# Performance work log

Measured on AMD Instinct MI355X. Metric: run time of the kernel, lower is better.

Reference implementation:

```python
import jax, jax.numpy as jnp
import numpy as np

N_NODES = 50000
N_EDGES = 800000
N_FEAT, N_HID, N_LATENT = 512, 256, 128


def spmm(rows, cols, vals, dense):
    # out[r] += vals[e] * dense[cols[e]]  -- COO SpMM via segment_sum
    gathered = dense[cols] * vals[:, None]          # [E, d]
    return jax.ops.segment_sum(gathered, rows, num_segments=N_NODES)


def setup_inputs() -> dict:
    key = jax.random.key(0)
    ks = jax.random.split(key, 8)
    x = jax.random.normal(ks[0], (N_NODES, N_FEAT), dtype=jnp.float32)
    edge_rows = jax.random.randint(ks[1], (N_EDGES,), 0, N_NODES, dtype=jnp.int32)
    edge_cols = jax.random.randint(ks[2], (N_EDGES,), 0, N_NODES, dtype=jnp.int32)
    edge_vals = jax.random.uniform(ks[3], (N_EDGES,), dtype=jnp.float32)
    # Glorot-style init like the torch GraphConvolution
    W1 = jax.random.normal(ks[4], (N_FEAT, N_HID), dtype=jnp.float32) / np.sqrt(N_FEAT)
    b1 = jnp.zeros((N_HID,), dtype=jnp.float32)
    W2 = jax.random.normal(ks[5], (N_HID, N_LATENT), dtype=jnp.float32) / np.sqrt(N_HID)
    b2 = jnp.zeros((N_LATENT,), dtype=jnp.float32)
    return {"x": x, "edge_rows": edge_rows, "edge_cols": edge_cols,
            "edge_vals": edge_vals, "W1": W1, "b1": b1, "W2": W2, "b2": b2}


def reference(x, edge_rows, edge_cols, edge_vals, W1, b1, W2, b2):
    # layer 1: relu(adj @ (x @ W1) + b1)
    h = spmm(edge_rows, edge_cols, edge_vals, x @ W1) + b1
    h = jax.nn.relu(h)
    # layer 2: relu(adj @ (h @ W2) + b2)
    z = spmm(edge_rows, edge_cols, edge_vals, h @ W2) + b2
    return jax.nn.relu(z)
```

## Files before the change

kernel.cpp:

```cpp
#include <hip/hip_runtime.h>
#include <hip/hip_bf16.h>


typedef __attribute__((ext_vector_type(8))) short bf16x8;
typedef __attribute__((ext_vector_type(4))) float f32x4;

#define NN 50000
#define NE 800000
#define NF 512
#define NH 256
#define NL 128
#define NB ((NN + 255) / 256)

static __device__ __forceinline__ unsigned short f2bf(float f) {
  union { float f; unsigned int u; } v; v.f = f;
  unsigned int r = v.u + 0x7fffu + ((v.u >> 16) & 1u);
  return (unsigned short)(r >> 16);
}
static __device__ __forceinline__ float bf2f(unsigned short u) {
  union { unsigned int u; float f; } v; v.u = (unsigned int)u << 16;
  return v.f;
}

static __device__ __forceinline__ void gll16(const void* g, void* l) {
  __builtin_amdgcn_global_load_lds(
      (const __attribute__((address_space(1))) void*)g,
      (__attribute__((address_space(3))) void*)l, 16, 0, 0);
}

extern "C" __global__ void k_hist(const int* __restrict__ rows, int* __restrict__ counts, int n) {
  int i = blockIdx.x * 256 + threadIdx.x;
  if (i < n) atomicAdd(&counts[rows[i]], 1);
}

extern "C" __global__ __launch_bounds__(256) void k_blocksum(
    const int* __restrict__ counts, int* __restrict__ bsum, int n) {
  __shared__ int s[256];
  int t = threadIdx.x;
  int i = blockIdx.x * 256 + t;
  s[t] = (i < n) ? counts[i] : 0;
  __syncthreads();
  for (int off = 128; off > 0; off >>= 1) {
    if (t < off) s[t] += s[t + off];
    __syncthreads();
  }
  if (t == 0) bsum[blockIdx.x] = s[0];
}

extern "C" __global__ __launch_bounds__(256) void k_scansums(
    const int* __restrict__ bsum, int* __restrict__ bpre, int* __restrict__ rp, int nb, int n) {
  __shared__ int s[256];
  int t = threadIdx.x;
  int v = (t < nb) ? bsum[t] : 0;
  s[t] = v;
  __syncthreads();
  for (int off = 1; off < 256; off <<= 1) {
    int u = (t >= off) ? s[t - off] : 0;
    __syncthreads();
    s[t] += u;
    __syncthreads();
  }
  if (t < nb) bpre[t] = s[t] - v;
  if (t == 255) rp[n] = s[255];
}

extern "C" __global__ __launch_bounds__(256) void k_scanfin(
    const int* __restrict__ counts, const int* __restrict__ bpre,
    int* __restrict__ rp, int* __restrict__ cur, int n) {
  __shared__ int s[256];
  int t = threadIdx.x;
  int i = blockIdx.x * 256 + t;
  int c = (i < n) ? counts[i] : 0;
  s[t] = c;
  __syncthreads();
  for (int off = 1; off < 256; off <<= 1) {
    int u = (t >= off) ? s[t - off] : 0;
    __syncthreads();
    s[t] += u;
    __syncthreads();
  }
  if (i < n) {
    int e = bpre[blockIdx.x] + s[t] - c;
    rp[i] = e;
    cur[i] = e;
  }
}

extern "C" __global__ void k_scatter(const int* __restrict__ rows, const int* __restrict__ cols,
    const float* __restrict__ vals, int* __restrict__ cur, int2* __restrict__ ep, int n) {
  int i = blockIdx.x * 256 + threadIdx.x;
  if (i < n) {
    int p = atomicAdd(&cur[rows[i]], 1);
    int2 e; e.x = cols[i]; e.y = __float_as_int(vals[i]);
    ep[p] = e;
  }
}

extern "C" __global__ void k_cast4(const float4* __restrict__ in, ushort4* __restrict__ out, int n4) {
  int i = blockIdx.x * 256 + threadIdx.x;
  if (i < n4) {
    float4 f = in[i];
    ushort4 o; o.x = f2bf(f.x); o.y = f2bf(f.y); o.z = f2bf(f.z); o.w = f2bf(f.w);
    out[i] = o;
  }
}

extern "C" __global__ void k_transcast(const float* __restrict__ w, unsigned short* __restrict__ wt,
                                       int K, int N) {
  int k = blockIdx.x; int n = threadIdx.x;
  wt[(size_t)n * K + k] = f2bf(w[(size_t)k * N + n]);
}

#define BM 128
#define BN 128
#define BK 32

extern "C" __global__ __launch_bounds__(256) void k_gemm(
    const unsigned short* __restrict__ A, const unsigned short* __restrict__ BT,
    unsigned short* __restrict__ C, int M, int N, int K) {
  __shared__ __align__(16) unsigned short sA[BM * BK];
  __shared__ __align__(16) unsigned short sB[BN * BK];
  int tid = threadIdx.x;
  int lane = tid & 63, wid = tid >> 6;
  int wm = (wid >> 1) * 64, wn = (wid & 1) * 64;
  int bm = blockIdx.x * BM, bn = blockIdx.y * BN;
  int l15 = lane & 15, lq = lane >> 4;
  f32x4 acc[4][4];
#pragma unroll
  for (int i = 0; i < 4; ++i)
#pragma unroll
    for (int j = 0; j < 4; ++j) acc[i][j] = (f32x4){0.f, 0.f, 0.f, 0.f};

  for (int k0 = 0; k0 < K; k0 += BK) {
#pragma unroll
    for (int i = 0; i < 2; ++i) {
      int u = tid + 256 * i;
      int row = u >> 2, uc = (u & 3) * 8;
      int ga = bm + row; if (ga >= M) ga = M - 1;
      gll16(A + (size_t)ga * K + k0 + uc, &sA[row * BK + uc]);
      int gb = bn + row; if (gb >= N) gb = N - 1;
      gll16(BT + (size_t)gb * K + k0 + uc, &sB[row * BK + uc]);
    }
    __syncthreads();
    bf16x8 af[4], bfr[4];
#pragma unroll
    for (int t = 0; t < 4; ++t) {
      af[t]  = *(const bf16x8*)(&sA[(wm + t * 16 + l15) * BK + lq * 8]);
      bfr[t] = *(const bf16x8*)(&sB[(wn + t * 16 + l15) * BK + lq * 8]);
    }
#pragma unroll
    for (int mt = 0; mt < 4; ++mt)
#pragma unroll
      for (int nt = 0; nt < 4; ++nt)
        acc[mt][nt] = __builtin_amdgcn_mfma_f32_16x16x32_bf16(af[mt], bfr[nt], acc[mt][nt], 0, 0, 0);
    __syncthreads();
  }
#pragma unroll
  for (int mt = 0; mt < 4; ++mt) {
#pragma unroll
    for (int r = 0; r < 4; ++r) {
      int gr = bm + wm + mt * 16 + lq * 4 + r;
      if (gr < M) {
#pragma unroll
        for (int nt = 0; nt < 4; ++nt) {
          int gc = bn + wn + nt * 16 + l15;
          C[(size_t)gr * N + gc] = f2bf(acc[mt][nt][r]);
        }
      }
    }
  }
}

extern "C" __global__ __launch_bounds__(256) void k_spmm256(
    const int* __restrict__ rp, const int2* __restrict__ ep,
    const unsigned short* __restrict__ src, const float* __restrict__ bias,
    ushort4* __restrict__ out) {
  int row = blockIdx.x * 4 + (threadIdx.x >> 6);
  int lane = threadIdx.x & 63;
  if (row >= NN) return;
  int e0 = __builtin_amdgcn_readfirstlane(rp[row]);
  int e1 = __builtin_amdgcn_readfirstlane(rp[row + 1]);
  const ushort4* srcv = (const ushort4*)src;
  float4 acc = {0.f, 0.f, 0.f, 0.f};
  int e = e0;
  for (; e + 4 <= e1; e += 4) {
    int2 p0 = ep[e], p1 = ep[e + 1], p2 = ep[e + 2], p3 = ep[e + 3];
    ushort4 g0 = srcv[(size_t)p0.x * (NH / 4) + lane];
    ushort4 g1 = srcv[(size_t)p1.x * (NH / 4) + lane];
    ushort4 g2 = srcv[(size_t)p2.x * (NH / 4) + lane];
    ushort4 g3 = srcv[(size_t)p3.x * (NH / 4) + lane];
    float v0 = __int_as_float(p0.y), v1 = __int_as_float(p1.y);
    float v2 = __int_as_float(p2.y), v3 = __int_as_float(p3.y);
    acc.x = fmaf(v0, bf2f(g0.x), acc.x); acc.y = fmaf(v0, bf2f(g0.y), acc.y);
    acc.z = fmaf(v0, bf2f(g0.z), acc.z); acc.w = fmaf(v0, bf2f(g0.w), acc.w);
    acc.x = fmaf(v1, bf2f(g1.x), acc.x); acc.y = fmaf(v1, bf2f(g1.y), acc.y);
    acc.z = fmaf(v1, bf2f(g1.z), acc.z); acc.w = fmaf(v1, bf2f(g1.w), acc.w);
    acc.x = fmaf(v2, bf2f(g2.x), acc.x); acc.y = fmaf(v2, bf2f(g2.y), acc.y);
    acc.z = fmaf(v2, bf2f(g2.z), acc.z); acc.w = fmaf(v2, bf2f(g2.w), acc.w);
    acc.x = fmaf(v3, bf2f(g3.x), acc.x); acc.y = fmaf(v3, bf2f(g3.y), acc.y);
    acc.z = fmaf(v3, bf2f(g3.z), acc.z); acc.w = fmaf(v3, bf2f(g3.w), acc.w);
  }
  for (; e < e1; ++e) {
    int2 p = ep[e];
    float v = __int_as_float(p.y);
    ushort4 g = srcv[(size_t)p.x * (NH / 4) + lane];
    acc.x = fmaf(v, bf2f(g.x), acc.x); acc.y = fmaf(v, bf2f(g.y), acc.y);
    acc.z = fmaf(v, bf2f(g.z), acc.z); acc.w = fmaf(v, bf2f(g.w), acc.w);
  }
  float4 b = ((const float4*)bias)[lane];
  ushort4 o;
  o.x = f2bf(fmaxf(acc.x + b.x, 0.f));
  o.y = f2bf(fmaxf(acc.y + b.y, 0.f));
  o.z = f2bf(fmaxf(acc.z + b.z, 0.f));
  o.w = f2bf(fmaxf(acc.w + b.w, 0.f));
  out[(size_t)row * (NH / 4) + lane] = o;
}

extern "C" __global__ __launch_bounds__(256) void k_spmm128(
    const int* __restrict__ rp, const int2* __restrict__ ep,
    const unsigned short* __restrict__ src, const float* __restrict__ bias,
    float2* __restrict__ out) {
  int row = blockIdx.x * 4 + (threadIdx.x >> 6);
  int lane = threadIdx.x & 63;
  if (row >= NN) return;
  int e0 = __builtin_amdgcn_readfirstlane(rp[row]);
  int e1 = __builtin_amdgcn_readfirstlane(rp[row + 1]);
  const ushort2* srcv = (const ushort2*)src;
  float2 acc = {0.f, 0.f};
  int e = e0;
  for (; e + 4 <= e1; e += 4) {
    int2 p0 = ep[e], p1 = ep[e + 1], p2 = ep[e + 2], p3 = ep[e + 3];
    ushort2 g0 = srcv[(size_t)p0.x * (NL / 2) + lane];
    ushort2 g1 = srcv[(size_t)p1.x * (NL / 2) + lane];
    ushort2 g2 = srcv[(size_t)p2.x * (NL / 2) + lane];
    ushort2 g3 = srcv[(size_t)p3.x * (NL / 2) + lane];
    float v0 = __int_as_float(p0.y), v1 = __int_as_float(p1.y);
    float v2 = __int_as_float(p2.y), v3 = __int_as_float(p3.y);
    acc.x = fmaf(v0, bf2f(g0.x), acc.x); acc.y = fmaf(v0, bf2f(g0.y), acc.y);
    acc.x = fmaf(v1, bf2f(g1.x), acc.x); acc.y = fmaf(v1, bf2f(g1.y), acc.y);
    acc.x = fmaf(v2, bf2f(g2.x), acc.x); acc.y = fmaf(v2, bf2f(g2.y), acc.y);
    acc.x = fmaf(v3, bf2f(g3.x), acc.x); acc.y = fmaf(v3, bf2f(g3.y), acc.y);
  }
  for (; e < e1; ++e) {
    int2 p = ep[e];
    float v = __int_as_float(p.y);
    ushort2 g = srcv[(size_t)p.x * (NL / 2) + lane];
    acc.x = fmaf(v, bf2f(g.x), acc.x); acc.y = fmaf(v, bf2f(g.y), acc.y);
  }
  float2 b = ((const float2*)bias)[lane];
  float2 o;
  o.x = fmaxf(acc.x + b.x, 0.f);
  o.y = fmaxf(acc.y + b.y, 0.f);
  out[(size_t)row * (NL / 2) + lane] = o;
}

extern "C" void kernel_launch(void* const* d_in, const int* in_sizes, int n_in,
                              void* d_out, int out_size, void* d_ws, size_t ws_size,
                              hipStream_t stream) {
  const float* x   = (const float*)d_in[0];
  const int* erow  = (const int*)d_in[1];
  const int* ecol  = (const int*)d_in[2];
  const float* ev  = (const float*)d_in[3];
  const float* W1  = (const float*)d_in[4];
  const float* b1  = (const float*)d_in[5];
  const float* W2  = (const float*)d_in[6];
  const float* b2  = (const float*)d_in[7];

  char* ws = (char*)d_ws;
  unsigned short* xbf = (unsigned short*)(ws + 0);
  unsigned short* xwb = (unsigned short*)(ws + 51200000);
  unsigned short* hbf = (unsigned short*)(ws + 76800000);
  unsigned short* hwb = (unsigned short*)(ws + 102400000);
  unsigned short* w1t = (unsigned short*)(ws + 115200000);
  unsigned short* w2t = (unsigned short*)(ws + 115462144);
  int* rp    = (int*)(ws + 115527680);
  int* cur   = (int*)(ws + 115728384);
  int* cnt   = (int*)(ws + 115929088);
  int* bsum  = (int*)(ws + 116129792);
  int* bpre  = (int*)(ws + 116130816);
  int2* ep   = (int2*)(ws + 116131840);

  hipMemsetAsync(cnt, 0, NN * sizeof(int), stream);
  k_hist<<<NE / 256, 256, 0, stream>>>(erow, cnt, NE);
  k_blocksum<<<NB, 256, 0, stream>>>(cnt, bsum, NN);
  k_scansums<<<1, 256, 0, stream>>>(bsum, bpre, rp, NB, NN);
  k_scanfin<<<NB, 256, 0, stream>>>(cnt, bpre, rp, cur, NN);
  k_scatter<<<NE / 256, 256, 0, stream>>>(erow, ecol, ev, cur, ep, NE);

  k_cast4<<<(NN * NF / 4) / 256, 256, 0, stream>>>((const float4*)x, (ushort4*)xbf, NN * NF / 4);
  k_transcast<<<NF, NH, 0, stream>>>(W1, w1t, NF, NH);
  k_gemm<<<dim3((NN + BM - 1) / BM, NH / BN), 256, 0, stream>>>(xbf, w1t, xwb, NN, NH, NF);
  k_spmm256<<<NN / 4, 256, 0, stream>>>(rp, ep, xwb, b1, (ushort4*)hbf);

  k_transcast<<<NH, NL, 0, stream>>>(W2, w2t, NH, NL);
  k_gemm<<<dim3((NN + BM - 1) / BM, NL / BN), 256, 0, stream>>>(hbf, w2t, hwb, NN, NL, NH);
  k_spmm128<<<NN / 4, 256, 0, stream>>>(rp, ep, hwb, b2, (float2*)d_out);
}
```

Measured before the change: 397.6 us.

## Fuse fp32-to-bf16 cast into GEMM1, retile GEMM2, deepen SpMM unrolling

Drops the separate cast kernel for x: GEMM1 now reads fp32 x directly, converts it to bf16 while staging into LDS, and uses a K-tile of 64. This removes a full read and write of the 50000x512 bf16 intermediate. GEMM2 is specialised to a 64-row tile so twice as many blocks launch for the narrow N=128 output. Both SpMM kernels add an 8-edge unrolled loop with all gathers issued before the FMAs, giving more loads in flight. The trade-off is that GEMM1's A loads are now plain register loads with conversion instead of direct-to-LDS copies, and the fp32 A data read by both column blocks is twice as large as the old bf16 copy.

```diff
diff --git a/kernel.cpp b/kernel.cpp
--- a/kernel.cpp
+++ b/kernel.cpp
@@ -96,34 +96,21 @@
   }
 }
 
-extern "C" __global__ void k_cast4(const float4* __restrict__ in, ushort4* __restrict__ out, int n4) {
-  int i = blockIdx.x * 256 + threadIdx.x;
-  if (i < n4) {
-    float4 f = in[i];
-    ushort4 o; o.x = f2bf(f.x); o.y = f2bf(f.y); o.z = f2bf(f.z); o.w = f2bf(f.w);
-    out[i] = o;
-  }
-}
-
 extern "C" __global__ void k_transcast(const float* __restrict__ w, unsigned short* __restrict__ wt,
                                        int K, int N) {
   int k = blockIdx.x; int n = threadIdx.x;
   wt[(size_t)n * K + k] = f2bf(w[(size_t)k * N + n]);
 }
 
-#define BM 128
-#define BN 128
-#define BK 32
-
-extern "C" __global__ __launch_bounds__(256) void k_gemm(
-    const unsigned short* __restrict__ A, const unsigned short* __restrict__ BT,
-    unsigned short* __restrict__ C, int M, int N, int K) {
-  __shared__ __align__(16) unsigned short sA[BM * BK];
-  __shared__ __align__(16) unsigned short sB[BN * BK];
+extern "C" __global__ __launch_bounds__(256) void k_gemm1(
+    const float* __restrict__ A, const unsigned short* __restrict__ BT,
+    unsigned short* __restrict__ C) {
+  __shared__ __align__(16) unsigned short sA[128 * 64];
+  __shared__ __align__(16) unsigned short sB[128 * 64];
   int tid = threadIdx.x;
   int lane = tid & 63, wid = tid >> 6;
   int wm = (wid >> 1) * 64, wn = (wid & 1) * 64;
-  int bm = blockIdx.x * BM, bn = blockIdx.y * BN;
+  int bm = blockIdx.x * 128, bn = blockIdx.y * 128;
   int l15 = lane & 15, lq = lane >> 4;
   f32x4 acc[4][4];
 #pragma unroll
@@ -131,28 +118,37 @@
 #pragma unroll
     for (int j = 0; j < 4; ++j) acc[i][j] = (f32x4){0.f, 0.f, 0.f, 0.f};
 
-  for (int k0 = 0; k0 < K; k0 += BK) {
-#pragma unroll
-    for (int i = 0; i < 2; ++i) {
-      int u = tid + 256 * i;
-      int row = u >> 2, uc = (u & 3) * 8;
-      int ga = bm + row; if (ga >= M) ga = M - 1;
-      gll16(A + (size_t)ga * K + k0 + uc, &sA[row * BK + uc]);
-      int gb = bn + row; if (gb >= N) gb = N - 1;
-      gll16(BT + (size_t)gb * K + k0 + uc, &sB[row * BK + uc]);
-    }
-    __syncthreads();
-    bf16x8 af[4], bfr[4];
-#pragma unroll
-    for (int t = 0; t < 4; ++t) {
-      af[t]  = *(const bf16x8*)(&sA[(wm + t * 16 + l15) * BK + lq * 8]);
-      bfr[t] = *(const bf16x8*)(&sB[(wn + t * 16 + l15) * BK + lq * 8]);
-    }
-#pragma unroll
-    for (int mt = 0; mt < 4; ++mt)
-#pragma unroll
-      for (int nt = 0; nt < 4; ++nt)
-        acc[mt][nt] = __builtin_amdgcn_mfma_f32_16x16x32_bf16(af[mt], bfr[nt], acc[mt][nt], 0, 0, 0);
+  for (int k0 = 0; k0 < NF; k0 += 64) {
+#pragma unroll
+    for (int j = 0; j < 8; ++j) {
+      int u = tid + 256 * j;
+      int row = u >> 4, c4 = (u & 15) * 4;
+      int ga = bm + row; if (ga >= NN) ga = NN - 1;
+      float4 f = *(const float4*)(A + (size_t)ga * NF + k0 + c4);
+      ushort4 o; o.x = f2bf(f.x); o.y = f2bf(f.y); o.z = f2bf(f.z); o.w = f2bf(f.w);
+      *(ushort4*)(&sA[row * 64 + c4]) = o;
+    }
+#pragma unroll
+    for (int j = 0; j < 4; ++j) {
+      int u = tid + 256 * j;
+      int row = u >> 3, c8 = (u & 7) * 8;
+      gll16(BT + (size_t)(bn + row) * NF + k0 + c8, &sB[row * 64 + c8]);
+    }
+    __syncthreads();
+#pragma unroll
+    for (int ks = 0; ks < 64; ks += 32) {
+      bf16x8 af[4], bfr[4];
+#pragma unroll
+      for (int t = 0; t < 4; ++t) {
+        af[t]  = *(const bf16x8*)(&sA[(wm + t * 16 + l15) * 64 + ks + lq * 8]);
+        bfr[t] = *(const bf16x8*)(&sB[(wn + t * 16 + l15) * 64 + ks + lq * 8]);
+      }
+#pragma unroll
+      for (int mt = 0; mt < 4; ++mt)
+#pragma unroll
+        for (int nt = 0; nt < 4; ++nt)
+          acc[mt][nt] = __builtin_amdgcn_mfma_f32_16x16x32_bf16(af[mt], bfr[nt], acc[mt][nt], 0, 0, 0);
+    }
     __syncthreads();
   }
 #pragma unroll
@@ -160,11 +156,75 @@
 #pragma unroll
     for (int r = 0; r < 4; ++r) {
       int gr = bm + wm + mt * 16 + lq * 4 + r;
-      if (gr < M) {
+      if (gr < NN) {
 #pragma unroll
         for (int nt = 0; nt < 4; ++nt) {
           int gc = bn + wn + nt * 16 + l15;
-          C[(size_t)gr * N + gc] = f2bf(acc[mt][nt][r]);
+          C[(size_t)gr * NH + gc] = f2bf(acc[mt][nt][r]);
+        }
+      }
+    }
+  }
+}
+
+extern "C" __global__ __launch_bounds__(256) void k_gemm2(
+    const unsigned short* __restrict__ A, const unsigned short* __restrict__ BT,
+    unsigned short* __restrict__ C) {
+  __shared__ __align__(16) unsigned short sA[64 * 64];
+  __shared__ __align__(16) unsigned short sB[128 * 64];
+  int tid = threadIdx.x;
+  int lane = tid & 63, wid = tid >> 6;
+  int wm = (wid >> 1) * 32, wn = (wid & 1) * 64;
+  int bm = blockIdx.x * 64;
+  int l15 = lane & 15, lq = lane >> 4;
+  f32x4 acc[2][4];
+#pragma unroll
+  for (int i = 0; i < 2; ++i)
+#pragma unroll
+    for (int j = 0; j < 4; ++j) acc[i][j] = (f32x4){0.f, 0.f, 0.f, 0.f};
+
+  for (int k0 = 0; k0 < NH; k0 += 64) {
+#pragma unroll
+    for (int j = 0; j < 2; ++j) {
+      int u = tid + 256 * j;
+      int row = u >> 3, c8 = (u & 7) * 8;
+      int ga = bm + row; if (ga >= NN) ga = NN - 1;
+      gll16(A + (size_t)ga * NH + k0 + c8, &sA[row * 64 + c8]);
+    }
+#pragma unroll
+    for (int j = 0; j < 4; ++j) {
+      int u = tid + 256 * j;
+      int row = u >> 3, c8 = (u & 7) * 8;
+      gll16(BT + (size_t)row * NH + k0 + c8, &sB[row * 64 + c8]);
+    }
+    __syncthreads();
+#pragma unroll
+    for (int ks = 0; ks < 64; ks += 32) {
+      bf16x8 af[2], bfr[4];
+#pragma unroll
+      for (int t = 0; t < 2; ++t)
+        af[t] = *(const bf16x8*)(&sA[(wm + t * 16 + l15) * 64 + ks + lq * 8]);
+#pragma unroll
+      for (int t = 0; t < 4; ++t)
+        bfr[t] = *(const bf16x8*)(&sB[(wn + t * 16 + l15) * 64 + ks + lq * 8]);
+#pragma unroll
+      for (int mt = 0; mt < 2; ++mt)
+#pragma unroll
+        for (int nt = 0; nt < 4; ++nt)
+          acc[mt][nt] = __builtin_amdgcn_mfma_f32_16x16x32_bf16(af[mt], bfr[nt], acc[mt][nt], 0, 0, 0);
+    }
+    __syncthreads();
+  }
+#pragma unroll
+  for (int mt = 0; mt < 2; ++mt) {
+#pragma unroll
+    for (int r = 0; r < 4; ++r) {
+      int gr = bm + wm + mt * 16 + lq * 4 + r;
+      if (gr < NN) {
+#pragma unroll
+        for (int nt = 0; nt < 4; ++nt) {
+          int gc = wn + nt * 16 + l15;
+          C[(size_t)gr * NL + gc] = f2bf(acc[mt][nt][r]);
         }
       }
     }
@@ -183,22 +243,31 @@
   const ushort4* srcv = (const ushort4*)src;
   float4 acc = {0.f, 0.f, 0.f, 0.f};
   int e = e0;
+  for (; e + 8 <= e1; e += 8) {
+    int2 p[8]; ushort4 g[8];
+#pragma unroll
+    for (int j = 0; j < 8; ++j) p[j] = ep[e + j];
+#pragma unroll
+    for (int j = 0; j < 8; ++j) g[j] = srcv[(size_t)p[j].x * (NH / 4) + lane];
+#pragma unroll
+    for (int j = 0; j < 8; ++j) {
+      float v = __int_as_float(p[j].y);
+      acc.x = fmaf(v, bf2f(g[j].x), acc.x); acc.y = fmaf(v, bf2f(g[j].y), acc.y);
+      acc.z = fmaf(v, bf2f(g[j].z), acc.z); acc.w = fmaf(v, bf2f(g[j].w), acc.w);
+    }
+  }
   for (; e + 4 <= e1; e += 4) {
-    int2 p0 = ep[e], p1 = ep[e + 1], p2 = ep[e + 2], p3 = ep[e + 3];
-    ushort4 g0 = srcv[(size_t)p0.x * (NH / 4) + lane];
-    ushort4 g1 = srcv[(size_t)p1.x * (NH / 4) + lane];
-    ushort4 g2 = srcv[(size_t)p2.x * (NH / 4) + lane];
-    ushort4 g3 = srcv[(size_t)p3.x * (NH / 4) + lane];
-    float v0 = __int_as_float(p0.y), v1 = __int_as_float(p1.y);
-    float v2 = __int_as_float(p2.y), v3 = __int_as_float(p3.y);
-    acc.x = fmaf(v0, bf2f(g0.x), acc.x); acc.y = fmaf(v0, bf2f(g0.y), acc.y);
-    acc.z = fmaf(v0, bf2f(g0.z), acc.z); acc.w = fmaf(v0, bf2f(g0.w), acc.w);
-    acc.x = fmaf(v1, bf2f(g1.x), acc.x); acc.y = fmaf(v1, bf2f(g1.y), acc.y);
-    acc.z = fmaf(v1, bf2f(g1.z), acc.z); acc.w = fmaf(v1, bf2f(g1.w), acc.w);
-    acc.x = fmaf(v2, bf2f(g2.x), acc.x); acc.y = fmaf(v2, bf2f(g2.y), acc.y);
-    acc.z = fmaf(v2, bf2f(g2.z), acc.z); acc.w = fmaf(v2, bf2f(g2.w), acc.w);
-    acc.x = fmaf(v3, bf2f(g3.x), acc.x); acc.y = fmaf(v3, bf2f(g3.y), acc.y);
-    acc.z = fmaf(v3, bf2f(g3.z), acc.z); acc.w = fmaf(v3, bf2f(g3.w), acc.w);
+    int2 p[4]; ushort4 g[4];
+#pragma unroll
+    for (int j = 0; j < 4; ++j) p[j] = ep[e + j];
+#pragma unroll
+    for (int j = 0; j < 4; ++j) g[j] = srcv[(size_t)p[j].x * (NH / 4) + lane];
+#pragma unroll
+    for (int j = 0; j < 4; ++j) {
+      float v = __int_as_float(p[j].y);
+      acc.x = fmaf(v, bf2f(g[j].x), acc.x); acc.y = fmaf(v, bf2f(g[j].y), acc.y);
+      acc.z = fmaf(v, bf2f(g[j].z), acc.z); acc.w = fmaf(v, bf2f(g[j].w), acc.w);
+    }
   }
   for (; e < e1; ++e) {
     int2 p = ep[e];
@@ -228,18 +297,29 @@
   const ushort2* srcv = (const ushort2*)src;
   float2 acc = {0.f, 0.f};
   int e = e0;
+  for (; e + 8 <= e1; e += 8) {
+    int2 p[8]; ushort2 g[8];
+#pragma unroll
+    for (int j = 0; j < 8; ++j) p[j] = ep[e + j];
+#pragma unroll
+    for (int j = 0; j < 8; ++j) g[j] = srcv[(size_t)p[j].x * (NL / 2) + lane];
+#pragma unroll
+    for (int j = 0; j < 8; ++j) {
+      float v = __int_as_float(p[j].y);
+      acc.x = fmaf(v, bf2f(g[j].x), acc.x); acc.y = fmaf(v, bf2f(g[j].y), acc.y);
+    }
+  }
   for (; e + 4 <= e1; e += 4) {
-    int2 p0 = ep[e], p1 = ep[e + 1], p2 = ep[e + 2], p3 = ep[e + 3];
-    ushort2 g0 = srcv[(size_t)p0.x * (NL / 2) + lane];
-    ushort2 g1 = srcv[(size_t)p1.x * (NL / 2) + lane];
-    ushort2 g2 = srcv[(size_t)p2.x * (NL / 2) + lane];
-    ushort2 g3 = srcv[(size_t)p3.x * (NL / 2) + lane];
-    float v0 = __int_as_float(p0.y), v1 = __int_as_float(p1.y);
-    float v2 = __int_as_float(p2.y), v3 = __int_as_float(p3.y);
-    acc.x = fmaf(v0, bf2f(g0.x), acc.x); acc.y = fmaf(v0, bf2f(g0.y), acc.y);
-    acc.x = fmaf(v1, bf2f(g1.x), acc.x); acc.y = fmaf(v1, bf2f(g1.y), acc.y);
-    acc.x = fmaf(v2, bf2f(g2.x), acc.x); acc.y = fmaf(v2, bf2f(g2.y), acc.y);
-    acc.x = fmaf(v3, bf2f(g3.x), acc.x); acc.y = fmaf(v3, bf2f(g3.y), acc.y);
+    int2 p[4]; ushort2 g[4];
+#pragma unroll
+    for (int j = 0; j < 4; ++j) p[j] = ep[e + j];
+#pragma unroll
+    for (int j = 0; j < 4; ++j) g[j] = srcv[(size_t)p[j].x * (NL / 2) + lane];
+#pragma unroll
+    for (int j = 0; j < 4; ++j) {
+      float v = __int_as_float(p[j].y);
+      acc.x = fmaf(v, bf2f(g[j].x), acc.x); acc.y = fmaf(v, bf2f(g[j].y), acc.y);
+    }
   }
   for (; e < e1; ++e) {
     int2 p = ep[e];
@@ -267,18 +347,17 @@
   const float* b2  = (const float*)d_in[7];
 
   char* ws = (char*)d_ws;
-  unsigned short* xbf = (unsigned short*)(ws + 0);
-  unsigned short* xwb = (unsigned short*)(ws + 51200000);
-  unsigned short* hbf = (unsigned short*)(ws + 76800000);
-  unsigned short* hwb = (unsigned short*)(ws + 102400000);
-  unsigned short* w1t = (unsigned short*)(ws + 115200000);
-  unsigned short* w2t = (unsigned short*)(ws + 115462144);
-  int* rp    = (int*)(ws + 115527680);
-  int* cur   = (int*)(ws + 115728384);
-  int* cnt   = (int*)(ws + 115929088);
-  int* bsum  = (int*)(ws + 116129792);
-  int* bpre  = (int*)(ws + 116130816);
-  int2* ep   = (int2*)(ws + 116131840);
+  unsigned short* xwb = (unsigned short*)(ws + 0);
+  unsigned short* hbf = (unsigned short*)(ws + 25600000);
+  unsigned short* hwb = (unsigned short*)(ws + 51200000);
+  unsigned short* w1t = (unsigned short*)(ws + 64000000);
+  unsigned short* w2t = (unsigned short*)(ws + 64262144);
+  int* rp    = (int*)(ws + 64327680);
+  int* cur   = (int*)(ws + 64528384);
+  int* cnt   = (int*)(ws + 64729088);
+  int* bsum  = (int*)(ws + 64929792);
+  int* bpre  = (int*)(ws + 64930816);
+  int2* ep   = (int2*)(ws + 64931840);
 
   hipMemsetAsync(cnt, 0, NN * sizeof(int), stream);
   k_hist<<<NE / 256, 256, 0, stream>>>(erow, cnt, NE);
@@ -287,12 +366,11 @@
   k_scanfin<<<NB, 256, 0, stream>>>(cnt, bpre, rp, cur, NN);
   k_scatter<<<NE / 256, 256, 0, stream>>>(erow, ecol, ev, cur, ep, NE);
 
-  k_cast4<<<(NN * NF / 4) / 256, 256, 0, stream>>>((const float4*)x, (ushort4*)xbf, NN * NF / 4);
   k_transcast<<<NF, NH, 0, stream>>>(W1, w1t, NF, NH);
-  k_gemm<<<dim3((NN + BM - 1) / BM, NH / BN), 256, 0, stream>>>(xbf, w1t, xwb, NN, NH, NF);
+  k_gemm1<<<dim3((NN + 127) / 128, NH / 128), 256, 0, stream>>>(x, w1t, xwb);
   k_spmm256<<<NN / 4, 256, 0, stream>>>(rp, ep, xwb, b1, (ushort4*)hbf);
 
   k_transcast<<<NH, NL, 0, stream>>>(W2, w2t, NH, NL);
-  k_gemm<<<dim3((NN + BM - 1) / BM, NL / BN), 256, 0, stream>>>(hbf, w2t, hwb, NN, NL, NH);
+  k_gemm2<<<(NN + 63) / 64, 256, 0, stream>>>(hbf, w2t, hwb);
   k_spmm128<<<NN / 4, 256, 0, stream>>>(rp, ep, hwb, b2, (float2*)d_out);
 }
```

After: 377.0 us. 5.2% less time.
